# Kernel optimization log

Measured on AMD Instinct MI355X. Metric: run time of the kernel, lower is better.

Reference implementation:

```python
import jax, jax.numpy as jnp
import numpy as np

N = 4096
M = 1024
APPERTURE = 250
L1, L2, L3, PRED = 1024, 512, 128, 1
EPS = 1e-6


def _layer_norm(x, gamma, beta):
    # torch x.std(-1) is unbiased (ddof=1)
    mean = jnp.mean(x, axis=-1, keepdims=True)
    std = jnp.std(x, axis=-1, ddof=1, keepdims=True)
    return gamma * (x - mean) / (std + EPS) + beta


def _self_attention(x, Wq, Wk, Wv, Wo, band_mask):
    # x: [n, m]; Linear(bias=False) => x @ W.T
    K = x @ Wk.T
    Q = (x @ Wq.T) * 0.06
    V = x @ Wv.T
    logits = Q @ K.T                      # [n, n]
    logits = jnp.where(band_mask, logits, -jnp.inf)  # keep |i-j| < apperture
    att = jax.nn.softmax(logits, axis=-1)
    # original: y = (V^T @ att)^T == att^T @ V  (note the transpose!)
    y = att.T @ V
    return y @ Wo.T, att


def setup_inputs() -> dict:
    key = jax.random.key(0)
    ks = jax.random.split(key, 20)
    s = 0.02
    inp = {
        'x1': jax.random.normal(ks[0], (1, N, M), jnp.float32),
        'x2': jax.random.normal(ks[1], (1, N, M), jnp.float32),
        'x3': jax.random.normal(ks[2], (1, N, M), jnp.float32),
        'Wq': jax.random.normal(ks[3], (M, M), jnp.float32) * s,
        'Wk': jax.random.normal(ks[4], (M, M), jnp.float32) * s,
        'Wv': jax.random.normal(ks[5], (M, M), jnp.float32) * s,
        'Wo': jax.random.normal(ks[6], (M, M), jnp.float32) * s,
        'ka_w': jax.random.normal(ks[7], (L1, M), jnp.float32) * s,
        'ka_b': jnp.zeros((L1,), jnp.float32),
        'kb_w': jax.random.normal(ks[8], (L2, L1), jnp.float32) * s,
        'kb_b': jnp.zeros((L2,), jnp.float32),
        'kc_w': jax.random.normal(ks[9], (L3, L2), jnp.float32) * s,
        'kc_b': jnp.zeros((L3,), jnp.float32),
        'kd_w': jax.random.normal(ks[10], (PRED, L3), jnp.float32) * s,
        'kd_b': jnp.zeros((PRED,), jnp.float32),
        'g13': jnp.ones((M,), jnp.float32),
        'b13': jnp.zeros((M,), jnp.float32),
        'gkc': jnp.ones((L3,), jnp.float32),
        'bkc': jnp.zeros((L3,), jnp.float32),
        'seq_len': N,
    }
    return inp


def reference(x1, x2, x3, Wq, Wk, Wv, Wo, ka_w, ka_b, kb_w, kb_b, kc_w, kc_b,
              kd_w, kd_b, g13, b13, gkc, bkc, seq_len):
    x1 = x1.reshape(-1, x1.shape[2])
    x2 = x2.reshape(-1, x2.shape[2])
    x3 = x3.reshape(-1, x3.shape[2])
    n = x1.shape[0]
    idx = jnp.arange(n)
    band_mask = jnp.abs(idx[:, None] - idx[None, :]) < APPERTURE  # allowed

    y1, att1 = _self_attention(x1, Wq, Wk, Wv, Wo, band_mask)
    y2, _ = _self_attention(x2, Wq, Wk, Wv, Wo, band_mask)
    y3, _ = _self_attention(x3, Wq, Wk, Wv, Wo, band_mask)

    # residual + (dropout == identity in eval) + shared LayerNorm
    y1 = _layer_norm(y1 + x1, g13, b13)
    y2 = _layer_norm(y2 + x2, g13, b13)
    y3 = _layer_norm(y3 + x3, g13, b13)

    y = y1 + y2 + y3  # cmb == [1,1,1]
    y = y @ ka_w.T + ka_b
    y = y @ kb_w.T + kb_b
    y = jax.nn.relu(y @ kc_w.T + kc_b)
    y = _layer_norm(y, gkc, bkc)
    y = jax.nn.sigmoid(y @ kd_w.T + kd_b)
    return y.reshape(1, -1), att1
```

## Files before the change

kernel.cpp:

```cpp
#include <hip/hip_runtime.h>
#include <hip/hip_bf16.h>
#include <cstdint>
#include <cstddef>

#define NSEQ 4096
#define MDIM 1024

typedef __attribute__((ext_vector_type(8))) short short8;
typedef __attribute__((ext_vector_type(4))) float f32x4;
typedef __attribute__((ext_vector_type(2))) long long2v;

typedef const __attribute__((address_space(1))) void gvoid_t;
typedef __attribute__((address_space(3))) void lvoid_t;

__device__ __forceinline__ unsigned short f2b(float x) {
  union { float f; unsigned int u; } a; a.f = x;
  unsigned int r = (a.u + 0x7fffu + ((a.u >> 16) & 1u)) >> 16;
  return (unsigned short)r;
}
__device__ __forceinline__ float b2f(unsigned short u) {
  union { float f; unsigned int u32; } a; a.u32 = ((unsigned int)u) << 16;
  return a.f;
}
__device__ __forceinline__ unsigned char f2e4(float x) {
  return (unsigned char)(__builtin_amdgcn_cvt_pk_fp8_f32(x, x, 0, false) & 0xff);
}
__device__ __forceinline__ unsigned int f2e4x4(float a, float b, float c, float d) {
  unsigned int lo = __builtin_amdgcn_cvt_pk_fp8_f32(a, b, 0, false);
  return (unsigned int)__builtin_amdgcn_cvt_pk_fp8_f32(c, d, lo, true);
}

__global__ __launch_bounds__(256) void k_cvt_all(
    const float* __restrict__ s0, const float* __restrict__ s1,
    const float* __restrict__ s2, const float* __restrict__ s3,
    const float* __restrict__ s4, const float* __restrict__ s5,
    const float* __restrict__ s6,
    const float* __restrict__ xa, const float* __restrict__ xb,
    const float* __restrict__ xc,
    unsigned char* __restrict__ Wf8, unsigned short* __restrict__ Wmlp,
    unsigned char* __restrict__ Xdst) {
  int idx = blockIdx.x * 256 + threadIdx.x;
  if (idx < 1048576) {
    int seg = idx >> 18, local = idx & 262143;
    const float* src = (seg == 0) ? s0 : (seg == 1) ? s1 : (seg == 2) ? s2 : s3;
    float4 v = *(const float4*)(src + (size_t)local * 4);
    *(unsigned int*)(Wf8 + (size_t)idx * 4) =
        f2e4x4(v.x * 64.f, v.y * 64.f, v.z * 64.f, v.w * 64.f);
  } else if (idx < 1458176) {
    int i2 = idx - 1048576;
    const float* src; int local;
    if (i2 < 262144) { src = s4; local = i2; }
    else if (i2 < 393216) { src = s5; local = i2 - 262144; }
    else { src = s6; local = i2 - 393216; }
    float4 v = *(const float4*)(src + (size_t)local * 4);
    ushort4 o; o.x = f2b(v.x); o.y = f2b(v.y); o.z = f2b(v.z); o.w = f2b(v.w);
    *(ushort4*)(Wmlp + (size_t)i2 * 4) = o;
  } else {
    int i2 = idx - 1458176;
    int seg = i2 >> 20, local = i2 & 1048575;
    const float* src = (seg == 0) ? xa : (seg == 1) ? xb : xc;
    float4 v = *(const float4*)(src + (size_t)local * 4);
    *(unsigned int*)(Xdst + (size_t)i2 * 4) = f2e4x4(v.x, v.y, v.z, v.w);
  }
}

__global__ __launch_bounds__(256) void k_gemm(
    const unsigned char* __restrict__ A, int lda,
    const unsigned char* __restrict__ B, int ldb,
    void* __restrict__ Cout, void* __restrict__ Cout2, int ldc,
    int K, float alpha,
    const float* __restrict__ bias, int relu, int okind, int do_exp, int mode,
    const unsigned char* __restrict__ A1, const unsigned char* __restrict__ A2) {
  __shared__ unsigned char smem[2 * 128 * 128];
  unsigned char* As = smem;
  unsigned char* Bs = smem + 128 * 128;
  int bx = blockIdx.x, by = blockIdx.y;
  const unsigned char* Ab;
  const unsigned char* Bb;
  void* Cdst = Cout;
  int k0 = 0, k1 = K, a_koff = 0;
  int ldce = ldc;
  int crow0 = bx * 128, ccol0 = by * 128;
  if (mode == 0) {
    Ab = A + (size_t)bx * 128 * lda;
    Bb = B + (size_t)by * 128 * ldb;
  } else if (mode == 3) {
    if (by < 16) {
      Ab = A + (size_t)bx * 128 * lda;
      Bb = B + (size_t)by * 128 * ldb;
      if (by >= 8) Cdst = Cout2;
      ccol0 = (by & 7) * 128;
    } else {
      Ab = A1 + (size_t)(by - 16) * 128 * 1024;
      Bb = A + (size_t)bx * 128 * lda;
      Cdst = (void*)const_cast<unsigned char*>(A2);
      crow0 = (by - 16) * 128; ccol0 = bx * 128;
      ldce = 3 * NSEQ;
    }
  } else if (mode == 1) {
    int s = bx >> 5, ti = bx & 31;
    int bt = ti + by - 2;
    if (bt < 0 || bt >= 32) return;
    Ab = A + (size_t)bx * 128 * lda;
    Bb = B + (size_t)(s * 32 + bt) * 128 * ldb;
  } else {
    int s = bx >> 5, ti = bx & 31;
    const unsigned char* Abase = (s == 0) ? A : ((s == 1) ? A1 : A2);
    Ab = Abase + (size_t)ti * 128 * lda;
    int lo = ti - 2; if (lo < 0) lo = 0;
    int hi = ti + 3; if (hi > 32) hi = 32;
    k0 = lo * 128; k1 = hi * 128;
    a_koff = (ti - 2) * 128;
    Bb = B + (size_t)by * 128 * ldb + s * NSEQ;
  }

  const int t = threadIdx.x;
  const int l = t & 63;
  const int w = t >> 6;
  const int fr = l & 15;
  const int quad = l >> 4;
  const int wm = (w >> 1) * 64;
  const int wn = (w & 1) * 64;
  const int fq4 = quad * 4;

  int srow[4], scg[4], sloff[4];
#pragma unroll
  for (int j = 0; j < 4; j++) {
    srow[j] = w * 32 + j * 8 + (l >> 3);
    scg[j] = ((l & 7) - srow[j]) & 7;
    sloff[j] = (w * 32 + j * 8) * 128 + l * 16;
  }

  f32x4 acc[4][4];
#pragma unroll
  for (int m = 0; m < 4; m++)
#pragma unroll
    for (int n = 0; n < 4; n++) acc[m][n] = (f32x4){0.f, 0.f, 0.f, 0.f};

  for (int kk = k0; kk < k1; kk += 128) {
    int ka = kk - a_koff;
    __syncthreads();
#pragma unroll
    for (int j = 0; j < 4; j++)
      __builtin_amdgcn_global_load_lds(
          (gvoid_t*)(Ab + (size_t)srow[j] * lda + ka + scg[j] * 16),
          (lvoid_t*)(As + sloff[j]), 16, 0, 0);
#pragma unroll
    for (int j = 0; j < 4; j++)
      __builtin_amdgcn_global_load_lds(
          (gvoid_t*)(Bb + (size_t)srow[j] * ldb + kk + scg[j] * 16),
          (lvoid_t*)(Bs + sloff[j]), 16, 0, 0);
    __syncthreads();
#pragma unroll
    for (int kb2 = 0; kb2 < 2; kb2++) {
      long2v a16[4], b16[4];
      int cq = quad * 2 + kb2;
#pragma unroll
      for (int m = 0; m < 4; m++) {
        int r = wm + m * 16 + fr;
        int slot = (cq + r) & 7;
        a16[m] = *(const long2v*)(As + r * 128 + slot * 16);
      }
#pragma unroll
      for (int n = 0; n < 4; n++) {
        int r = wn + n * 16 + fr;
        int slot = (cq + r) & 7;
        b16[n] = *(const long2v*)(Bs + r * 128 + slot * 16);
      }
#pragma unroll
      for (int m = 0; m < 4; m++)
#pragma unroll
        for (int n = 0; n < 4; n++)
          acc[m][n] = __builtin_amdgcn_mfma_f32_16x16x32_fp8_fp8(a16[m].x, b16[n].x, acc[m][n], 0, 0, 0);
#pragma unroll
      for (int m = 0; m < 4; m++)
#pragma unroll
        for (int n = 0; n < 4; n++)
          acc[m][n] = __builtin_amdgcn_mfma_f32_16x16x32_fp8_fp8(a16[m].y, b16[n].y, acc[m][n], 0, 0, 0);
    }
  }

  if (okind == 1) {
    __syncthreads();
    unsigned short* sm16 = (unsigned short*)smem;
#pragma unroll
    for (int m = 0; m < 4; m++) {
#pragma unroll
      for (int n = 0; n < 4; n++) {
        int colb = wn + n * 16 + fr;
        float bv = bias ? bias[ccol0 + colb] : 0.f;
#pragma unroll
        for (int r = 0; r < 4; r++) {
          int row = wm + m * 16 + fq4 + r;
          float v = acc[m][n][r] * alpha + bv;
          if (do_exp) v = __expf(v);
          if (relu) v = fmaxf(v, 0.f);
          int cc = ((colb >> 3) + row) & 15;
          sm16[row * 128 + cc * 8 + (colb & 7)] = f2b(v);
        }
      }
    }
    __syncthreads();
    unsigned short* Cp = (unsigned short*)Cdst;
    for (int i = t; i < 2048; i += 256) {
      int row = i >> 4, lc = i & 15;
      int pc = (lc + row) & 15;
      uint4 v = *(const uint4*)(sm16 + row * 128 + pc * 8);
      *(uint4*)(Cp + (size_t)(crow0 + row) * ldce + ccol0 + lc * 8) = v;
    }
  } else if (okind == 2) {
    __syncthreads();
#pragma unroll
    for (int m = 0; m < 4; m++) {
#pragma unroll
      for (int n = 0; n < 4; n++) {
        int colb = wn + n * 16 + fr;
        float bv = bias ? bias[ccol0 + colb] : 0.f;
#pragma unroll
        for (int r = 0; r < 4; r++) {
          int row = wm + m * 16 + fq4 + r;
          float v = acc[m][n][r] * alpha + bv;
          if (relu) v = fmaxf(v, 0.f);
          int sl = ((colb >> 4) + row) & 7;
          smem[row * 128 + sl * 16 + (colb & 15)] = f2e4(v);
        }
      }
    }
    __syncthreads();
    unsigned char* Cp = (unsigned char*)Cdst;
    for (int i = t; i < 1024; i += 256) {
      int row = i >> 3, lc = i & 7;
      int pc = (lc + row) & 7;
      uint4 v = *(const uint4*)(smem + row * 128 + pc * 16);
      *(uint4*)(Cp + (size_t)(crow0 + row) * ldce + ccol0 + lc * 16) = v;
    }
  } else {
    float* Cp = (float*)Cdst;
#pragma unroll
    for (int m = 0; m < 4; m++) {
#pragma unroll
      for (int n = 0; n < 4; n++) {
        int colb = wn + n * 16 + fr;
        float bv = bias ? bias[ccol0 + colb] : 0.f;
#pragma unroll
        for (int r = 0; r < 4; r++) {
          int row = wm + m * 16 + fq4 + r;
          float v = acc[m][n][r] * alpha + bv;
          if (relu) v = fmaxf(v, 0.f);
          Cp[(size_t)(crow0 + row) * ldce + ccol0 + colb] = v;
        }
      }
    }
  }
}

__global__ __launch_bounds__(256) void k_gemm64(
    const unsigned short* __restrict__ A, int lda,
    const unsigned short* __restrict__ B, int ldb,
    void* __restrict__ Cout, int ldc, int K,
    const float* __restrict__ bias, int relu, int out_bf16) {
  __shared__ unsigned short smem[2 * 64 * 64];
  unsigned short* As = smem;
  unsigned short* Bs = smem + 64 * 64;
  int bx = blockIdx.x, by = blockIdx.y;
  const unsigned short* Ab = A + (size_t)bx * 64 * lda;
  const unsigned short* Bb = B + (size_t)by * 64 * ldb;
  int crow0 = bx * 64, ccol0 = by * 64;

  const int t = threadIdx.x;
  const int l = t & 63;
  const int w = t >> 6;
  const int fr = l & 15;
  const int quad = l >> 4;
  const int wm = (w & 1) * 32;
  const int wn = (w >> 1) * 32;
  const int fq4 = quad * 4;

  int srow[2], scg[2], sloff[2];
#pragma unroll
  for (int j = 0; j < 2; j++) {
    srow[j] = w * 16 + j * 8 + (l >> 3);
    scg[j] = ((l & 7) - srow[j]) & 7;
    sloff[j] = (w * 16 + j * 8) * 64 + l * 8;
  }

  f32x4 acc[2][2];
#pragma unroll
  for (int m = 0; m < 2; m++)
#pragma unroll
    for (int n = 0; n < 2; n++) acc[m][n] = (f32x4){0.f, 0.f, 0.f, 0.f};

  for (int kk = 0; kk < K; kk += 64) {
    __syncthreads();
#pragma unroll
    for (int j = 0; j < 2; j++)
      __builtin_amdgcn_global_load_lds(
          (gvoid_t*)(Ab + (size_t)srow[j] * lda + kk + scg[j] * 8),
          (lvoid_t*)(As + sloff[j]), 16, 0, 0);
#pragma unroll
    for (int j = 0; j < 2; j++)
      __builtin_amdgcn_global_load_lds(
          (gvoid_t*)(Bb + (size_t)srow[j] * ldb + kk + scg[j] * 8),
          (lvoid_t*)(Bs + sloff[j]), 16, 0, 0);
    __syncthreads();
#pragma unroll
    for (int s = 0; s < 2; s++) {
      short8 af[2], bf[2];
#pragma unroll
      for (int m = 0; m < 2; m++) {
        int r = wm + m * 16 + fr;
        int slot = (s * 4 + quad + r) & 7;
        af[m] = *(const short8*)(As + r * 64 + slot * 8);
      }
#pragma unroll
      for (int n = 0; n < 2; n++) {
        int r = wn + n * 16 + fr;
        int slot = (s * 4 + quad + r) & 7;
        bf[n] = *(const short8*)(Bs + r * 64 + slot * 8);
      }
#pragma unroll
      for (int m = 0; m < 2; m++)
#pragma unroll
        for (int n = 0; n < 2; n++)
          acc[m][n] = __builtin_amdgcn_mfma_f32_16x16x32_bf16(af[m], bf[n], acc[m][n], 0, 0, 0);
    }
  }

  if (out_bf16) {
    __syncthreads();
#pragma unroll
    for (int m = 0; m < 2; m++) {
#pragma unroll
      for (int n = 0; n < 2; n++) {
        int colb = wn + n * 16 + fr;
        float bv = bias ? bias[ccol0 + colb] : 0.f;
#pragma unroll
        for (int r = 0; r < 4; r++) {
          int row = wm + m * 16 + fq4 + r;
          float v = acc[m][n][r] + bv;
          if (relu) v = fmaxf(v, 0.f);
          int cc = ((colb >> 3) + row) & 7;
          smem[row * 64 + cc * 8 + (colb & 7)] = f2b(v);
        }
      }
    }
    __syncthreads();
    unsigned short* Cp = (unsigned short*)Cout;
    for (int i = t; i < 512; i += 256) {
      int row = i >> 3, lc = i & 7;
      int pc = (lc + row) & 7;
      uint4 v = *(const uint4*)(smem + row * 64 + pc * 8);
      *(uint4*)(Cp + (size_t)(crow0 + row) * ldc + ccol0 + lc * 8) = v;
    }
  } else {
    float* Cp = (float*)Cout;
#pragma unroll
    for (int m = 0; m < 2; m++) {
#pragma unroll
      for (int n = 0; n < 2; n++) {
        int colb = wn + n * 16 + fr;
        float bv = bias ? bias[ccol0 + colb] : 0.f;
#pragma unroll
        for (int r = 0; r < 4; r++) {
          int row = wm + m * 16 + fq4 + r;
          float v = acc[m][n][r] + bv;
          if (relu) v = fmaxf(v, 0.f);
          Cp[(size_t)(crow0 + row) * ldc + ccol0 + colb] = v;
        }
      }
    }
  }
}

__global__ __launch_bounds__(256) void k_stats(const unsigned short* __restrict__ Eband,
                                               float* __restrict__ sums) {
  int ig = blockIdx.x * 4 + (threadIdx.x >> 6);
  int lane = threadIdx.x & 63;
  int i = ig & 4095;
  int ti = i >> 7;
  int cbase = (ti - 2) * 128;
  int jlo = i - 249; if (jlo < 0) jlo = 0;
  int jhi = i + 249; if (jhi > NSEQ - 1) jhi = NSEQ - 1;
  int clo = jlo - cbase, chi = jhi - cbase;
  const unsigned short* L = Eband + (size_t)ig * 640;
  float s = 0.f;
  for (int c = clo + lane; c <= chi; c += 64) s += b2f(L[c]);
  for (int off = 32; off; off >>= 1) s += __shfl_xor(s, off);
  if (lane == 0) sums[ig] = s;
}

__global__ __launch_bounds__(256) void k_build_attT(const unsigned short* __restrict__ Eband,
                                                    const float* __restrict__ sums,
                                                    unsigned char* __restrict__ t0,
                                                    unsigned char* __restrict__ t1,
                                                    unsigned char* __restrict__ t2) {
  int byy = blockIdx.y;
  int s = byy >> 5, ti = byy & 31;
  int tj = ti + (int)blockIdx.x - 2;
  if (tj < 0 || tj >= 32) return;
  unsigned char* dst = (s == 0) ? t0 : ((s == 1) ? t1 : t2);
  __shared__ unsigned char T[128][132];
  int t = threadIdx.x;
  int c0 = (ti - tj + 2) * 128;
  int colg = (t & 31) * 4;
  for (int jj = t >> 5; jj < 128; jj += 8) {
    int jg = s * NSEQ + tj * 128 + jj;
    float inv = 16.f / sums[jg];
    ushort4 v = *(const ushort4*)&Eband[(size_t)jg * 640 + c0 + colg];
    float vv[4] = {b2f(v.x), b2f(v.y), b2f(v.z), b2f(v.w)};
#pragma unroll
    for (int q = 0; q < 4; q++) {
      int i = ti * 128 + colg + q;
      int d = i - (tj * 128 + jj);
      float a = (d < 250 && d > -250) ? vv[q] * inv : 0.f;
      T[colg + q][jj] = f2e4(a);
    }
  }
  __syncthreads();
  int jb0 = (tj - ti + 2) * 128;
  for (int ii = t >> 5; ii < 128; ii += 8) {
    size_t o = (size_t)(ti * 128 + ii) * 640 + jb0 + colg;
    *(unsigned int*)(dst + o) = *(const unsigned int*)&T[ii][colg];
  }
}

__global__ __launch_bounds__(256) void k_write_att(const unsigned short* __restrict__ Eband,
                                                   const float* __restrict__ sums,
                                                   float* __restrict__ att) {
  int i = blockIdx.x;
  int ti = i >> 7, cbase = (ti - 2) * 128;
  int jlo = i - 249; if (jlo < 0) jlo = 0;
  int jhi = i + 249; if (jhi > NSEQ - 1) jhi = NSEQ - 1;
  float inv = 1.f / sums[i];
  const unsigned short* L = Eband + (size_t)i * 640;
  float* arow = att + (size_t)i * NSEQ;
  for (int j0 = threadIdx.x * 4; j0 < NSEQ; j0 += 1024) {
    float ov[4];
#pragma unroll
    for (int q = 0; q < 4; q++) {
      int j = j0 + q;
      ov[q] = (j >= jlo && j <= jhi) ? b2f(L[j - cbase]) * inv : 0.f;
    }
    *(float4*)(arow + j0) = make_float4(ov[0], ov[1], ov[2], ov[3]);
  }
}

__global__ __launch_bounds__(256) void k_ln3(const unsigned short* __restrict__ yo,
                                             const float* __restrict__ x1,
                                             const float* __restrict__ x2,
                                             const float* __restrict__ x3,
                                             const float* __restrict__ g,
                                             const float* __restrict__ b,
                                             unsigned short* __restrict__ ysum_b) {
  int i = blockIdx.x, t = threadIdx.x;
  int w = t >> 6, lane = t & 63;
  __shared__ float red[8];
  const float* xs[3] = {x1, x2, x3};
  float4 gg = *(const float4*)(g + t * 4);
  float4 bb = *(const float4*)(b + t * 4);
  float acc[4] = {0.f, 0.f, 0.f, 0.f};
  for (int s = 0; s < 3; s++) {
    ushort4 yv = *(const ushort4*)(yo + ((size_t)(s * NSEQ + i)) * MDIM + t * 4);
    float4 xx = *(const float4*)(xs[s] + (size_t)i * MDIM + t * 4);
    float v[4] = {b2f(yv.x) + xx.x, b2f(yv.y) + xx.y, b2f(yv.z) + xx.z, b2f(yv.w) + xx.w};
    float s1 = v[0] + v[1] + v[2] + v[3];
    float s2 = v[0]*v[0] + v[1]*v[1] + v[2]*v[2] + v[3]*v[3];
    for (int off = 32; off; off >>= 1) { s1 += __shfl_xor(s1, off); s2 += __shfl_xor(s2, off); }
    __syncthreads();
    if (lane == 0) { red[w] = s1; red[4 + w] = s2; }
    __syncthreads();
    float S1 = red[0] + red[1] + red[2] + red[3];
    float S2 = red[4] + red[5] + red[6] + red[7];
    float mean = S1 * (1.f / 1024.f);
    float var = (S2 - S1 * mean) * (1.f / 1023.f);
    float rstd = 1.f / (sqrtf(var) + 1e-6f);
    acc[0] += gg.x * (v[0] - mean) * rstd + bb.x;
    acc[1] += gg.y * (v[1] - mean) * rstd + bb.y;
    acc[2] += gg.z * (v[2] - mean) * rstd + bb.z;
    acc[3] += gg.w * (v[3] - mean) * rstd + bb.w;
  }
  ushort4 o;
  o.x = f2b(acc[0]); o.y = f2b(acc[1]); o.z = f2b(acc[2]); o.w = f2b(acc[3]);
  *(ushort4*)(ysum_b + (size_t)i * MDIM + t * 4) = o;
}

__global__ __launch_bounds__(128) void k_final(const float* __restrict__ h3,
                                               const float* __restrict__ g,
                                               const float* __restrict__ b,
                                               const float* __restrict__ kdw,
                                               const float* __restrict__ kdb,
                                               float* __restrict__ yout) {
  int i = blockIdx.x, t = threadIdx.x;
  float v = h3[(size_t)i * 128 + t];
  float s1 = v, s2 = v * v;
  for (int off = 32; off; off >>= 1) { s1 += __shfl_xor(s1, off); s2 += __shfl_xor(s2, off); }
  __shared__ float red[4];
  int w = t >> 6, lane = t & 63;
  if (lane == 0) { red[w] = s1; red[2 + w] = s2; }
  __syncthreads();
  float S1 = red[0] + red[1], S2 = red[2] + red[3];
  float mean = S1 * (1.f / 128.f);
  float var = (S2 - S1 * mean) * (1.f / 127.f);
  float rstd = 1.f / (sqrtf(var) + 1e-6f);
  float ln = g[t] * (v - mean) * rstd + b[t];
  float p = ln * kdw[t];
  for (int off = 32; off; off >>= 1) p += __shfl_xor(p, off);
  __syncthreads();
  if (lane == 0) red[w] = p;
  __syncthreads();
  if (t == 0) {
    float z = red[0] + red[1] + kdb[0];
    yout[i] = 1.f / (1.f + __expf(-z));
  }
}

extern "C" void kernel_launch(void* const* d_in, const int* in_sizes, int n_in,
                              void* d_out, int out_size, void* d_ws, size_t ws_size,
                              hipStream_t stream) {
  const float* x1 = (const float*)d_in[0];
  const float* x2 = (const float*)d_in[1];
  const float* x3 = (const float*)d_in[2];
  const float* Wq = (const float*)d_in[3];
  const float* Wk = (const float*)d_in[4];
  const float* Wv = (const float*)d_in[5];
  const float* Wo = (const float*)d_in[6];
  const float* ka_w = (const float*)d_in[7];
  const float* ka_b = (const float*)d_in[8];
  const float* kb_w = (const float*)d_in[9];
  const float* kb_b = (const float*)d_in[10];
  const float* kc_w = (const float*)d_in[11];
  const float* kc_b = (const float*)d_in[12];
  const float* kd_w = (const float*)d_in[13];
  const float* kd_b = (const float*)d_in[14];
  const float* g13 = (const float*)d_in[15];
  const float* b13 = (const float*)d_in[16];
  const float* gkc = (const float*)d_in[17];
  const float* bkc = (const float*)d_in[18];

  float* y_out = (float*)d_out;
  float* att_out = y_out + NSEQ;

  char* ws = (char*)d_ws;
  size_t off = 0;
  auto alloc = [&](size_t bytes) -> void* {
    void* p = ws + off;
    off += (bytes + 255) & ~(size_t)255;
    return p;
  };
  const size_t NM = (size_t)3 * NSEQ * MDIM;
  unsigned char* Wf = (unsigned char*)alloc(4 * 1048576);
  unsigned short* Wmlp = (unsigned short*)alloc((1048576 + 524288 + 65536) * 2);
  unsigned char* Xf = (unsigned char*)alloc(NM);
  unsigned char* Qf = (unsigned char*)alloc(NM);
  unsigned char* Kf = (unsigned char*)alloc(NM);
  unsigned char* VTf = (unsigned char*)alloc(NM);
  unsigned short* Eband = (unsigned short*)alloc((size_t)3 * NSEQ * 640 * 2);
  float* sums = (float*)alloc((size_t)3 * NSEQ * 4);
  unsigned char* aT0 = (unsigned char*)alloc((size_t)NSEQ * 640);
  unsigned char* aT1 = (unsigned char*)alloc((size_t)NSEQ * 640);
  unsigned char* aT2 = (unsigned char*)alloc((size_t)NSEQ * 640);
  unsigned char* Wv_f = Wf + 2097152;
  unsigned char* Wo_f = Wf + 3145728;
  unsigned short* ka_b16 = Wmlp;
  unsigned short* kb_b16 = Wmlp + 1048576;
  unsigned short* kc_b16 = Wmlp + 1572864;
  unsigned char* yb = Xf;
  unsigned short* yo = (unsigned short*)Qf;
  unsigned short* ysum_b = (unsigned short*)VTf;
  unsigned short* h1b = (unsigned short*)Xf;
  unsigned short* h2b = (unsigned short*)Qf;
  float* h3 = (float*)aT0;

  k_cvt_all<<<17984, 256, 0, stream>>>(Wq, Wk, Wv, Wo, ka_w, kb_w, kc_w,
                                       x1, x2, x3, Wf, Wmlp, Xf);

  k_gemm<<<dim3(96, 24), 256, 0, stream>>>(Xf, 1024, Wf, 1024, Qf, Kf, 1024,
                                           1024, 1.f / 64.f, nullptr, 0, 2, 0, 3,
                                           Wv_f, VTf);
  k_gemm<<<dim3(96, 5), 256, 0, stream>>>(Qf, 1024, Kf, 1024, Eband, nullptr, 640,
                                          1024, 0.06f, nullptr, 0, 1, 1, 1,
                                          nullptr, nullptr);
  k_stats<<<3072, 256, 0, stream>>>(Eband, sums);
  k_build_attT<<<dim3(5, 96), 256, 0, stream>>>(Eband, sums, aT0, aT1, aT2);
  k_gemm<<<dim3(96, 8), 256, 0, stream>>>(aT0, 640, VTf, 3 * NSEQ, yb, nullptr, 1024,
                                          NSEQ, 0.5f, nullptr, 0, 2, 0, 2,
                                          aT1, aT2);
  k_write_att<<<4096, 256, 0, stream>>>(Eband, sums, att_out);
  k_gemm<<<dim3(96, 8), 256, 0, stream>>>(yb, 1024, Wo_f, 1024, yo, nullptr, 1024,
                                          1024, 1.f / 512.f, nullptr, 0, 1, 0, 0,
                                          nullptr, nullptr);
  k_ln3<<<4096, 256, 0, stream>>>(yo, x1, x2, x3, g13, b13, ysum_b);

  k_gemm64<<<dim3(64, 16), 256, 0, stream>>>(ysum_b, 1024, ka_b16, 1024, h1b, 1024,
                                             1024, ka_b, 0, 1);
  k_gemm64<<<dim3(64, 8), 256, 0, stream>>>(h1b, 1024, kb_b16, 1024, h2b, 512,
                                            1024, kb_b, 0, 1);
  k_gemm64<<<dim3(64, 2), 256, 0, stream>>>(h2b, 512, kc_b16, 512, h3, 128,
                                            512, kc_b, 1, 0);
  k_final<<<4096, 128, 0, stream>>>(h3, gkc, bkc, kd_w, kd_b, y_out);
}
```

Measured before the change: 372.1 us.

## Swap GEMM operand roles so each lane stores contiguous output directly

```diff
diff --git a/kernel.cpp b/kernel.cpp
--- a/kernel.cpp
+++ b/kernel.cpp
@@ -68,8 +68,7 @@
     const unsigned char* __restrict__ A, int lda,
     const unsigned char* __restrict__ B, int ldb,
     void* __restrict__ Cout, void* __restrict__ Cout2, int ldc,
-    int K, float alpha,
-    const float* __restrict__ bias, int relu, int okind, int do_exp, int mode,
+    int K, float alpha, int okind, int do_exp, int mode,
     const unsigned char* __restrict__ A1, const unsigned char* __restrict__ A2) {
   __shared__ unsigned char smem[2 * 128 * 128];
   unsigned char* As = smem;
@@ -78,40 +77,45 @@
   const unsigned char* Ab;
   const unsigned char* Bb;
   void* Cdst = Cout;
-  int k0 = 0, k1 = K, a_koff = 0;
+  int k0 = 0, k1 = K, b_koff = 0;
   int ldce = ldc;
-  int crow0 = bx * 128, ccol0 = by * 128;
+  int rbase, cbase;
+  int ldae = lda, ldbe = ldb;
   if (mode == 0) {
-    Ab = A + (size_t)bx * 128 * lda;
-    Bb = B + (size_t)by * 128 * ldb;
+    Ab = A + (size_t)by * 128 * lda;
+    Bb = B + (size_t)bx * 128 * ldb;
+    rbase = bx * 128; cbase = by * 128;
   } else if (mode == 3) {
     if (by < 16) {
-      Ab = A + (size_t)bx * 128 * lda;
-      Bb = B + (size_t)by * 128 * ldb;
+      Ab = A + (size_t)by * 128 * lda;
+      Bb = B + (size_t)bx * 128 * ldb;
       if (by >= 8) Cdst = Cout2;
-      ccol0 = (by & 7) * 128;
+      rbase = bx * 128; cbase = (by & 7) * 128;
     } else {
-      Ab = A1 + (size_t)(by - 16) * 128 * 1024;
-      Bb = A + (size_t)bx * 128 * lda;
+      Ab = B + (size_t)bx * 128 * ldb;
+      Bb = A1 + (size_t)(by - 16) * 128 * 1024;
       Cdst = (void*)const_cast<unsigned char*>(A2);
-      crow0 = (by - 16) * 128; ccol0 = bx * 128;
+      rbase = (by - 16) * 128; cbase = bx * 128;
       ldce = 3 * NSEQ;
     }
   } else if (mode == 1) {
     int s = bx >> 5, ti = bx & 31;
     int bt = ti + by - 2;
     if (bt < 0 || bt >= 32) return;
-    Ab = A + (size_t)bx * 128 * lda;
-    Bb = B + (size_t)(s * 32 + bt) * 128 * ldb;
+    Ab = A + (size_t)(s * 32 + bt) * 128 * lda;
+    Bb = B + (size_t)bx * 128 * ldb;
+    rbase = bx * 128; cbase = by * 128;
   } else {
     int s = bx >> 5, ti = bx & 31;
-    const unsigned char* Abase = (s == 0) ? A : ((s == 1) ? A1 : A2);
-    Ab = Abase + (size_t)ti * 128 * lda;
+    Ab = A + (size_t)by * 128 * lda + s * NSEQ;
+    const unsigned char* Bbase = (s == 0) ? B : ((s == 1) ? A1 : A2);
+    Bb = Bbase + (size_t)ti * 128 * 640;
+    ldbe = 640;
     int lo = ti - 2; if (lo < 0) lo = 0;
     int hi = ti + 3; if (hi > 32) hi = 32;
     k0 = lo * 128; k1 = hi * 128;
-    a_koff = (ti - 2) * 128;
-    Bb = B + (size_t)by * 128 * ldb + s * NSEQ;
+    b_koff = (ti - 2) * 128;
+    rbase = bx * 128; cbase = by * 128;
   }
 
   const int t = threadIdx.x;
@@ -138,17 +142,17 @@
     for (int n = 0; n < 4; n++) acc[m][n] = (f32x4){0.f, 0.f, 0.f, 0.f};
 
   for (int kk = k0; kk < k1; kk += 128) {
-    int ka = kk - a_koff;
+    int kb = kk - b_koff;
     __syncthreads();
 #pragma unroll
     for (int j = 0; j < 4; j++)
       __builtin_amdgcn_global_load_lds(
-          (gvoid_t*)(Ab + (size_t)srow[j] * lda + ka + scg[j] * 16),
+          (gvoid_t*)(Ab + (size_t)srow[j] * ldae + kk + scg[j] * 16),
           (lvoid_t*)(As + sloff[j]), 16, 0, 0);
 #pragma unroll
     for (int j = 0; j < 4; j++)
       __builtin_amdgcn_global_load_lds(
-          (gvoid_t*)(Bb + (size_t)srow[j] * ldb + kk + scg[j] * 16),
+          (gvoid_t*)(Bb + (size_t)srow[j] * ldbe + kb + scg[j] * 16),
           (lvoid_t*)(Bs + sloff[j]), 16, 0, 0);
     __syncthreads();
 #pragma unroll
@@ -180,75 +184,23 @@
     }
   }
 
-  if (okind == 1) {
-    __syncthreads();
-    unsigned short* sm16 = (unsigned short*)smem;
-#pragma unroll
-    for (int m = 0; m < 4; m++) {
-#pragma unroll
-      for (int n = 0; n < 4; n++) {
-        int colb = wn + n * 16 + fr;
-        float bv = bias ? bias[ccol0 + colb] : 0.f;
-#pragma unroll
-        for (int r = 0; r < 4; r++) {
-          int row = wm + m * 16 + fq4 + r;
-          float v = acc[m][n][r] * alpha + bv;
-          if (do_exp) v = __expf(v);
-          if (relu) v = fmaxf(v, 0.f);
-          int cc = ((colb >> 3) + row) & 15;
-          sm16[row * 128 + cc * 8 + (colb & 7)] = f2b(v);
-        }
-      }
-    }
-    __syncthreads();
-    unsigned short* Cp = (unsigned short*)Cdst;
-    for (int i = t; i < 2048; i += 256) {
-      int row = i >> 4, lc = i & 15;
-      int pc = (lc + row) & 15;
-      uint4 v = *(const uint4*)(sm16 + row * 128 + pc * 8);
-      *(uint4*)(Cp + (size_t)(crow0 + row) * ldce + ccol0 + lc * 8) = v;
-    }
-  } else if (okind == 2) {
-    __syncthreads();
-#pragma unroll
-    for (int m = 0; m < 4; m++) {
-#pragma unroll
-      for (int n = 0; n < 4; n++) {
-        int colb = wn + n * 16 + fr;
-        float bv = bias ? bias[ccol0 + colb] : 0.f;
-#pragma unroll
-        for (int r = 0; r < 4; r++) {
-          int row = wm + m * 16 + fq4 + r;
-          float v = acc[m][n][r] * alpha + bv;
-          if (relu) v = fmaxf(v, 0.f);
-          int sl = ((colb >> 4) + row) & 7;
-          smem[row * 128 + sl * 16 + (colb & 15)] = f2e4(v);
-        }
-      }
-    }
-    __syncthreads();
-    unsigned char* Cp = (unsigned char*)Cdst;
-    for (int i = t; i < 1024; i += 256) {
-      int row = i >> 3, lc = i & 7;
-      int pc = (lc + row) & 7;
-      uint4 v = *(const uint4*)(smem + row * 128 + pc * 16);
-      *(uint4*)(Cp + (size_t)(crow0 + row) * ldce + ccol0 + lc * 16) = v;
-    }
-  } else {
-    float* Cp = (float*)Cdst;
-#pragma unroll
-    for (int m = 0; m < 4; m++) {
-#pragma unroll
-      for (int n = 0; n < 4; n++) {
-        int colb = wn + n * 16 + fr;
-        float bv = bias ? bias[ccol0 + colb] : 0.f;
-#pragma unroll
-        for (int r = 0; r < 4; r++) {
-          int row = wm + m * 16 + fq4 + r;
-          float v = acc[m][n][r] * alpha + bv;
-          if (relu) v = fmaxf(v, 0.f);
-          Cp[(size_t)(crow0 + row) * ldce + ccol0 + colb] = v;
-        }
+#pragma unroll
+  for (int m = 0; m < 4; m++) {
+#pragma unroll
+    for (int n = 0; n < 4; n++) {
+      int oc = cbase + wm + m * 16 + fq4;
+      int orow = rbase + wn + n * 16 + fr;
+      float v0 = acc[m][n][0] * alpha, v1 = acc[m][n][1] * alpha;
+      float v2 = acc[m][n][2] * alpha, v3 = acc[m][n][3] * alpha;
+      if (okind == 1) {
+        if (do_exp) { v0 = __expf(v0); v1 = __expf(v1); v2 = __expf(v2); v3 = __expf(v3); }
+        ushort4 o; o.x = f2b(v0); o.y = f2b(v1); o.z = f2b(v2); o.w = f2b(v3);
+        *(uint2*)((unsigned short*)Cdst + (size_t)orow * ldce + oc) = *(uint2*)&o;
+      } else if (okind == 2) {
+        *(unsigned int*)((unsigned char*)Cdst + (size_t)orow * ldce + oc) =
+            f2e4x4(v0, v1, v2, v3);
+      } else {
+        *(float4*)((float*)Cdst + (size_t)orow * ldce + oc) = make_float4(v0, v1, v2, v3);
       }
     }
   }
@@ -263,9 +215,9 @@
   unsigned short* As = smem;
   unsigned short* Bs = smem + 64 * 64;
   int bx = blockIdx.x, by = blockIdx.y;
-  const unsigned short* Ab = A + (size_t)bx * 64 * lda;
-  const unsigned short* Bb = B + (size_t)by * 64 * ldb;
-  int crow0 = bx * 64, ccol0 = by * 64;
+  const unsigned short* Ab = A + (size_t)by * 64 * lda;
+  const unsigned short* Bb = B + (size_t)bx * 64 * ldb;
+  int rbase = bx * 64, cbase = by * 64;
 
   const int t = threadIdx.x;
   const int l = t & 63;
@@ -326,47 +278,24 @@
     }
   }
 
-  if (out_bf16) {
-    __syncthreads();
-#pragma unroll
-    for (int m = 0; m < 2; m++) {
-#pragma unroll
-      for (int n = 0; n < 2; n++) {
-        int colb = wn + n * 16 + fr;
-        float bv = bias ? bias[ccol0 + colb] : 0.f;
-#pragma unroll
-        for (int r = 0; r < 4; r++) {
-          int row = wm + m * 16 + fq4 + r;
-          float v = acc[m][n][r] + bv;
-          if (relu) v = fmaxf(v, 0.f);
-          int cc = ((colb >> 3) + row) & 7;
-          smem[row * 64 + cc * 8 + (colb & 7)] = f2b(v);
-        }
-      }
-    }
-    __syncthreads();
-    unsigned short* Cp = (unsigned short*)Cout;
-    for (int i = t; i < 512; i += 256) {
-      int row = i >> 3, lc = i & 7;
-      int pc = (lc + row) & 7;
-      uint4 v = *(const uint4*)(smem + row * 64 + pc * 8);
-      *(uint4*)(Cp + (size_t)(crow0 + row) * ldc + ccol0 + lc * 8) = v;
-    }
-  } else {
-    float* Cp = (float*)Cout;
-#pragma unroll
-    for (int m = 0; m < 2; m++) {
-#pragma unroll
-      for (int n = 0; n < 2; n++) {
-        int colb = wn + n * 16 + fr;
-        float bv = bias ? bias[ccol0 + colb] : 0.f;
-#pragma unroll
-        for (int r = 0; r < 4; r++) {
-          int row = wm + m * 16 + fq4 + r;
-          float v = acc[m][n][r] + bv;
-          if (relu) v = fmaxf(v, 0.f);
-          Cp[(size_t)(crow0 + row) * ldc + ccol0 + colb] = v;
-        }
+#pragma unroll
+  for (int m = 0; m < 2; m++) {
+#pragma unroll
+    for (int n = 0; n < 2; n++) {
+      int oc = cbase + wm + m * 16 + fq4;
+      int orow = rbase + wn + n * 16 + fr;
+      float4 bv = bias ? *(const float4*)(bias + oc) : make_float4(0.f, 0.f, 0.f, 0.f);
+      float v0 = acc[m][n][0] + bv.x, v1 = acc[m][n][1] + bv.y;
+      float v2 = acc[m][n][2] + bv.z, v3 = acc[m][n][3] + bv.w;
+      if (relu) {
+        v0 = fmaxf(v0, 0.f); v1 = fmaxf(v1, 0.f);
+        v2 = fmaxf(v2, 0.f); v3 = fmaxf(v3, 0.f);
+      }
+      if (out_bf16) {
+        ushort4 o; o.x = f2b(v0); o.y = f2b(v1); o.z = f2b(v2); o.w = f2b(v3);
+        *(uint2*)((unsigned short*)Cout + (size_t)orow * ldc + oc) = *(uint2*)&o;
+      } else {
+        *(float4*)((float*)Cout + (size_t)orow * ldc + oc) = make_float4(v0, v1, v2, v3);
       }
     }
   }
@@ -574,28 +503,24 @@
   k_cvt_all<<<17984, 256, 0, stream>>>(Wq, Wk, Wv, Wo, ka_w, kb_w, kc_w,
                                        x1, x2, x3, Wf, Wmlp, Xf);
 
-  k_gemm<<<dim3(96, 24), 256, 0, stream>>>(Xf, 1024, Wf, 1024, Qf, Kf, 1024,
-                                           1024, 1.f / 64.f, nullptr, 0, 2, 0, 3,
-                                           Wv_f, VTf);
-  k_gemm<<<dim3(96, 5), 256, 0, stream>>>(Qf, 1024, Kf, 1024, Eband, nullptr, 640,
-                                          1024, 0.06f, nullptr, 0, 1, 1, 1,
-                                          nullptr, nullptr);
+  k_gemm<<<dim3(96, 24), 256, 0, stream>>>(Wf, 1024, Xf, 1024, Qf, Kf, 1024,
+                                           1024, 1.f / 64.f, 2, 0, 3, Wv_f, VTf);
+  k_gemm<<<dim3(96, 5), 256, 0, stream>>>(Kf, 1024, Qf, 1024, Eband, nullptr, 640,
+                                          1024, 0.06f, 1, 1, 1, nullptr, nullptr);
   k_stats<<<3072, 256, 0, stream>>>(Eband, sums);
   k_build_attT<<<dim3(5, 96), 256, 0, stream>>>(Eband, sums, aT0, aT1, aT2);
-  k_gemm<<<dim3(96, 8), 256, 0, stream>>>(aT0, 640, VTf, 3 * NSEQ, yb, nullptr, 1024,
-                                          NSEQ, 0.5f, nullptr, 0, 2, 0, 2,
-                                          aT1, aT2);
+  k_gemm<<<dim3(96, 8), 256, 0, stream>>>(VTf, 3 * NSEQ, aT0, 640, yb, nullptr, 1024,
+                                          NSEQ, 0.5f, 2, 0, 2, aT1, aT2);
   k_write_att<<<4096, 256, 0, stream>>>(Eband, sums, att_out);
-  k_gemm<<<dim3(96, 8), 256, 0, stream>>>(yb, 1024, Wo_f, 1024, yo, nullptr, 1024,
-                                          1024, 1.f / 512.f, nullptr, 0, 1, 0, 0,
-                                          nullptr, nullptr);
+  k_gemm<<<dim3(96, 8), 256, 0, stream>>>(Wo_f, 1024, yb, 1024, yo, nullptr, 1024,
+                                          1024, 1.f / 512.f, 1, 0, 0, nullptr, nullptr);
   k_ln3<<<4096, 256, 0, stream>>>(yo, x1, x2, x3, g13, b13, ysum_b);
 
-  k_gemm64<<<dim3(64, 16), 256, 0, stream>>>(ysum_b, 1024, ka_b16, 1024, h1b, 1024,
+  k_gemm64<<<dim3(64, 16), 256, 0, stream>>>(ka_b16, 1024, ysum_b, 1024, h1b, 1024,
                                              1024, ka_b, 0, 1);
-  k_gemm64<<<dim3(64, 8), 256, 0, stream>>>(h1b, 1024, kb_b16, 1024, h2b, 512,
+  k_gemm64<<<dim3(64, 8), 256, 0, stream>>>(kb_b16, 1024, h1b, 1024, h2b, 512,
                                             1024, kb_b, 0, 1);
-  k_gemm64<<<dim3(64, 2), 256, 0, stream>>>(h2b, 512, kc_b16, 512, h3, 128,
+  k_gemm64<<<dim3(64, 2), 256, 0, stream>>>(kc_b16, 512, h2b, 512, h3, 128,
                                             512, kc_b, 1, 0);
   k_final<<<4096, 128, 0, stream>>>(h3, gkc, bkc, kd_w, kd_b, y_out);
 }
```

Result: faster. 363.1 us (-2.4%).
